# Kernel optimization log

Measured on AMD Instinct MI355X. Metric: run time of the kernel, lower is better.

## Reference

```python
import jax, jax.numpy as jnp
import numpy as np

H = 6  # num_heads
D = 384  # embedding_dim


def _rot(seg, coord):
    # seg: [BN, H, T, L], coord: [BN, T]; rotate interleaved even/odd pairs
    L = seg.shape[-1]
    pairs = max(L // 2, 1)
    inv_freq = 1.0 / (10000.0 ** (jnp.arange(pairs, dtype=seg.dtype) / pairs))
    ang = coord[..., None] * inv_freq          # [BN, T, pairs]
    cos = jnp.cos(ang)[:, None]                # [BN, 1, T, pairs]
    sin = jnp.sin(ang)[:, None]
    even, odd = seg[..., 0::2], seg[..., 1::2]
    re = even * cos - odd * sin
    ro = even * sin + odd * cos
    return jnp.stack((re, ro), axis=-1).reshape(seg.shape)


def _apply_rope3(t, pos, chunk):
    # t: [BN, H, T, Hd], pos: [BN, T, 3]; three axis chunks, tail untouched
    parts, s = [], 0
    for i in range(3):
        parts.append(_rot(t[..., s:s + chunk], pos[..., i]))
        s += chunk
    parts.append(t[..., s:])
    return jnp.concatenate(parts, axis=-1)


def setup_inputs() -> dict:
    key = jax.random.key(0)
    ks = jax.random.split(key, 10)
    B, N, T = 8, 64, 128
    scale = 1.0 / np.sqrt(D)
    return {
        "padded_batches": jax.random.normal(ks[0], (B, N, T, D), jnp.float32),
        "sum_token": jax.random.normal(ks[1], (B, N, 1, D), jnp.float32),
        "positions_3d": jax.random.uniform(ks[2], (B, N, T, 3), jnp.float32),
        "Wq": jax.random.normal(ks[3], (D, D), jnp.float32) * scale,
        "bq": jax.random.normal(ks[4], (D,), jnp.float32) * scale,
        "Wk": jax.random.normal(ks[5], (D, D), jnp.float32) * scale,
        "bk": jax.random.normal(ks[6], (D,), jnp.float32) * scale,
        "Wv": jax.random.normal(ks[7], (D, D), jnp.float32) * scale,
        "bv": jax.random.normal(ks[8], (D,), jnp.float32) * scale,
        "masks": jax.random.randint(ks[9], (B, N, T), 0, 2, jnp.int32),
    }


def reference(padded_batches, sum_token, positions_3d, Wq, bq, Wk, bk, Wv, bv, masks):
    B, N, T, Dm = padded_batches.shape
    Hd = Dm // H
    chunk = Hd // 6 * 2

    # masked mean-pool summary token (summary_mode='avg')
    w = masks[..., None].astype(padded_batches.dtype)          # [B,N,T,1]
    denom = jnp.clip(w.sum(axis=-2, keepdims=True), 1e-6, None)
    summary = (padded_batches * w).sum(axis=-2, keepdims=True) / denom  # [B,N,1,D]

    q = (padded_batches @ Wq + bq).reshape(B * N, T, H, Hd).transpose(0, 2, 1, 3)  # [BN,H,T,Hd]
    k = (summary @ Wk + bk).reshape(B * N, 1, H, Hd).transpose(0, 2, 1, 3)         # [BN,H,1,Hd]
    v = (summary @ Wv + bv).reshape(B * N, 1, H, Hd).transpose(0, 2, 1, 3)

    # 3-axis RoPE on q (token positions) and k (pooled positions)
    pos_summary = (positions_3d * w).sum(axis=-2, keepdims=True) / denom  # [B,N,1,3]
    pos_q = positions_3d.reshape(B * N, T, 3)
    pos_k = pos_summary.reshape(B * N, 1, 3)
    q = _apply_rope3(q, pos_q, chunk)
    k = _apply_rope3(k, pos_k, chunk)

    # SDPA with T queries vs 1 key
    scores = jnp.einsum('bhtd,bhkd->bhtk', q, k) / np.float32(np.sqrt(Hd))  # [BN,H,T,1]
    mask_add = jnp.where(masks.reshape(B * N, 1, T, 1) == 0,
                         jnp.finfo(jnp.float32).min, 0.0)
    attn_w = jax.nn.softmax(scores + mask_add, axis=-1)
    attn = jnp.einsum('bhtk,bhkd->bhtd', attn_w, v)  # [BN,H,T,Hd]

    out = attn.transpose(0, 2, 1, 3).reshape(B, N, T, Dm) + padded_batches
    return out
```

## Files before the change

### kernel.cpp

```cpp
#include <hip/hip_runtime.h>


#define DM 384
#define TT 128
#define C4 96
#define BN_TOT 512

typedef float f32x4 __attribute__((ext_vector_type(4)));

__device__ __forceinline__ void nt_store4(float4* p, const float4 v) {
    __builtin_nontemporal_store(*(const f32x4*)&v, (f32x4*)p);
}

__global__ __launch_bounds__(384) void k_partial(
    const float* __restrict__ padded,
    const int*   __restrict__ masks,
    float*       __restrict__ ws_part,
    float*       __restrict__ ws_cnt)
{
    const int b  = blockIdx.x;
    const int bn = b >> 2;
    const int q  = b & 3;
    const int t  = threadIdx.x;
    const int c  = t % C4;
    const int rr = t / C4;

    __shared__ float  w_sh[32];
    __shared__ float4 part[4][C4];

    if (t < 32) w_sh[t] = (float)masks[bn * TT + q * 32 + t];
    __syncthreads();

    const float4* __restrict__ p4 =
        (const float4*)padded + (size_t)bn * TT * C4 + (size_t)q * 32 * C4;

    float4 acc = make_float4(0.f, 0.f, 0.f, 0.f);
    #pragma unroll
    for (int j = 0; j < 8; ++j) {
        const int   r = rr + 4 * j;
        const float w = w_sh[r];
        const float4 x = p4[r * C4 + c];
        acc.x += x.x * w; acc.y += x.y * w; acc.z += x.z * w; acc.w += x.w * w;
    }
    part[rr][c] = acc;
    __syncthreads();

    if (t < C4) {
        const float4 a0 = part[0][t], a1 = part[1][t];
        const float4 a2 = part[2][t], a3 = part[3][t];
        float4 s;
        s.x = (a0.x + a1.x) + (a2.x + a3.x);
        s.y = (a0.y + a1.y) + (a2.y + a3.y);
        s.z = (a0.z + a1.z) + (a2.z + a3.z);
        s.w = (a0.w + a1.w) + (a2.w + a3.w);
        ((float4*)(ws_part + ((size_t)bn * 4 + q) * DM))[t] = s;
    } else if (t == C4) {
        float s0 = 0.f, s1 = 0.f, s2 = 0.f, s3 = 0.f;
        #pragma unroll
        for (int i = 0; i < 8; ++i) {
            s0 += w_sh[i];      s1 += w_sh[8 + i];
            s2 += w_sh[16 + i]; s3 += w_sh[24 + i];
        }
        ws_cnt[bn * 4 + q] = (s0 + s1) + (s2 + s3);
    }
}

__global__ __launch_bounds__(384) void k_final_add(
    const float* __restrict__ padded,
    const float* __restrict__ ws_part,
    const float* __restrict__ ws_cnt,
    const float* __restrict__ Wv,
    const float* __restrict__ bv,
    float*       __restrict__ out)
{
    const int b  = blockIdx.x;
    const int bn = b >> 1;
    const int h  = b & 1;
    const int t  = threadIdx.x;
    const int c4 = t % 48;
    const int g8 = t / 48;

    __shared__ float  summ[DM];
    __shared__ float4 mpart[8][48];
    __shared__ float4 v_sh[48];

    {
        const float* __restrict__ pp = ws_part + (size_t)bn * 4 * DM;
        const float  s = (pp[t] + pp[DM + t]) + (pp[2 * DM + t] + pp[3 * DM + t]);
        const float* __restrict__ cc = ws_cnt + bn * 4;
        const float  cnt = (cc[0] + cc[1]) + (cc[2] + cc[3]);
        summ[t] = s * (1.0f / fmaxf(cnt, 1e-6f));
    }
    __syncthreads();

    {
        float4 a = make_float4(0.f, 0.f, 0.f, 0.f);
        const float4* __restrict__ wv4 = (const float4*)Wv;
        #pragma unroll 6
        for (int j = 0; j < 48; ++j) {
            const int   e = g8 * 48 + j;
            const float s = summ[e];
            const float4 w = wv4[(size_t)e * C4 + h * 48 + c4];
            a.x += s * w.x; a.y += s * w.y; a.z += s * w.z; a.w += s * w.w;
        }
        mpart[g8][c4] = a;
    }
    __syncthreads();

    if (t < 48) {
        float4 v = ((const float4*)bv)[h * 48 + t];
        #pragma unroll
        for (int g = 0; g < 8; ++g) {
            const float4 p = mpart[g][t];
            v.x += p.x; v.y += p.y; v.z += p.z; v.w += p.w;
        }
        v_sh[t] = v;
    }
    __syncthreads();

    const float4* __restrict__ p4 = (const float4*)padded + (size_t)bn * TT * C4;
    float4*       __restrict__ o4 = (float4*)out + (size_t)bn * TT * C4;
    const float4 v = v_sh[c4];
    #pragma unroll
    for (int j = 0; j < 16; ++j) {
        const int    r   = g8 + 8 * j;
        const size_t idx = (size_t)r * C4 + h * 48 + c4;
        float4 x = p4[idx];
        x.x += v.x; x.y += v.y; x.z += v.z; x.w += v.w;
        nt_store4(&o4[idx], x);
    }
}

extern "C" void kernel_launch(void* const* d_in, const int* in_sizes, int n_in,
                              void* d_out, int out_size, void* d_ws, size_t ws_size,
                              hipStream_t stream) {
    const float* padded = (const float*)d_in[0];
    const float* Wv     = (const float*)d_in[7];
    const float* bv     = (const float*)d_in[8];
    const int*   masks  = (const int*)d_in[9];
    float* out = (float*)d_out;

    float* ws_part = (float*)d_ws;
    float* ws_cnt  = ws_part + (size_t)BN_TOT * 4 * DM;

    k_partial<<<BN_TOT * 4, 384, 0, stream>>>(padded, masks, ws_part, ws_cnt);
    k_final_add<<<BN_TOT * 2, 384, 0, stream>>>(padded, ws_part, ws_cnt,
                                                Wv, bv, out);
}
```

Measured before the change: 215.6 us.

## Fuse partial pooling and output add via last-block atomic counter

Merges the two kernels into one. Each of the four quarter-blocks for a sequence writes its partial masked sum, bumps an atomic counter, and the last block to arrive computes the summary, the V projection and the residual add for the whole sequence. Block indices are remapped so the four quarters of a sequence sit close together in launch order. This removes one kernel launch and the gap between launches, but adds a memset, atomics and fences, and leaves only a quarter of the blocks doing the full output pass serially.

```diff
diff --git a/kernel.cpp b/kernel.cpp
--- a/kernel.cpp
+++ b/kernel.cpp
@@ -5,6 +5,7 @@
 #define TT 128
 #define C4 96
 #define BN_TOT 512
+#define NBLK (BN_TOT * 4)
 
 typedef float f32x4 __attribute__((ext_vector_type(4)));
 
@@ -12,26 +13,34 @@
     __builtin_nontemporal_store(*(const f32x4*)&v, (f32x4*)p);
 }
 
-__global__ __launch_bounds__(384) void k_partial(
+__global__ __launch_bounds__(384) void fused_lastblock(
     const float* __restrict__ padded,
     const int*   __restrict__ masks,
-    float*       __restrict__ ws_part,
-    float*       __restrict__ ws_cnt)
+    const float* __restrict__ Wv,
+    const float* __restrict__ bv,
+    unsigned int* __restrict__ ws_cnt,
+    float*        __restrict__ ws_den,
+    float*        __restrict__ ws_part,
+    float*        __restrict__ out)
 {
-    const int b  = blockIdx.x;
-    const int bn = b >> 2;
-    const int q  = b & 3;
+    const int b = blockIdx.x;
+    const int q  = (b >> 3) & 3;
+    const int bn = ((b >> 5) << 3) | (b & 7);
+
     const int t  = threadIdx.x;
     const int c  = t % C4;
     const int rr = t / C4;
 
     __shared__ float  w_sh[32];
     __shared__ float4 part[4][C4];
+    __shared__ float  summ[DM];
+    __shared__ float  v_sh[DM];
+    __shared__ int    last_sh;
 
     if (t < 32) w_sh[t] = (float)masks[bn * TT + q * 32 + t];
     __syncthreads();
 
-    const float4* __restrict__ p4 =
+    const float4* __restrict__ p4q =
         (const float4*)padded + (size_t)bn * TT * C4 + (size_t)q * 32 * C4;
 
     float4 acc = make_float4(0.f, 0.f, 0.f, 0.f);
@@ -39,8 +48,9 @@
     for (int j = 0; j < 8; ++j) {
         const int   r = rr + 4 * j;
         const float w = w_sh[r];
-        const float4 x = p4[r * C4 + c];
-        acc.x += x.x * w; acc.y += x.y * w; acc.z += x.z * w; acc.w += x.w * w;
+        const float4 xv = p4q[r * C4 + c];
+        acc.x += xv.x * w; acc.y += xv.y * w;
+        acc.z += xv.z * w; acc.w += xv.w * w;
     }
     part[rr][c] = acc;
     __syncthreads();
@@ -61,73 +71,63 @@
             s0 += w_sh[i];      s1 += w_sh[8 + i];
             s2 += w_sh[16 + i]; s3 += w_sh[24 + i];
         }
-        ws_cnt[bn * 4 + q] = (s0 + s1) + (s2 + s3);
+        ws_den[bn * 4 + q] = (s0 + s1) + (s2 + s3);
     }
-}
 
-__global__ __launch_bounds__(384) void k_final_add(
-    const float* __restrict__ padded,
-    const float* __restrict__ ws_part,
-    const float* __restrict__ ws_cnt,
-    const float* __restrict__ Wv,
-    const float* __restrict__ bv,
-    float*       __restrict__ out)
-{
-    const int b  = blockIdx.x;
-    const int bn = b >> 1;
-    const int h  = b & 1;
-    const int t  = threadIdx.x;
-    const int c4 = t % 48;
-    const int g8 = t / 48;
+    __threadfence();
+    __syncthreads();
+    if (t == 0) {
+        const unsigned int old = atomicAdd(&ws_cnt[bn], 1u);
+        last_sh = (old == 3u);
+    }
+    __syncthreads();
+    if (!last_sh) return;
 
-    __shared__ float  summ[DM];
-    __shared__ float4 mpart[8][48];
-    __shared__ float4 v_sh[48];
+    __threadfence();
 
     {
         const float* __restrict__ pp = ws_part + (size_t)bn * 4 * DM;
         const float  s = (pp[t] + pp[DM + t]) + (pp[2 * DM + t] + pp[3 * DM + t]);
-        const float* __restrict__ cc = ws_cnt + bn * 4;
-        const float  cnt = (cc[0] + cc[1]) + (cc[2] + cc[3]);
-        summ[t] = s * (1.0f / fmaxf(cnt, 1e-6f));
+        const float* __restrict__ dd = ws_den + bn * 4;
+        const float  den = (dd[0] + dd[1]) + (dd[2] + dd[3]);
+        summ[t] = s * (1.0f / fmaxf(den, 1e-6f));
     }
     __syncthreads();
 
     {
         float4 a = make_float4(0.f, 0.f, 0.f, 0.f);
         const float4* __restrict__ wv4 = (const float4*)Wv;
-        #pragma unroll 6
-        for (int j = 0; j < 48; ++j) {
-            const int   e = g8 * 48 + j;
+        #pragma unroll 8
+        for (int j = 0; j < 96; ++j) {
+            const int   e = rr * 96 + j;
             const float s = summ[e];
-            const float4 w = wv4[(size_t)e * C4 + h * 48 + c4];
+            const float4 w = wv4[(size_t)e * C4 + c];
             a.x += s * w.x; a.y += s * w.y; a.z += s * w.z; a.w += s * w.w;
         }
-        mpart[g8][c4] = a;
+        part[rr][c] = a;
     }
     __syncthreads();
 
-    if (t < 48) {
-        float4 v = ((const float4*)bv)[h * 48 + t];
+    if (t < C4) {
+        float4 v = ((const float4*)bv)[t];
         #pragma unroll
-        for (int g = 0; g < 8; ++g) {
-            const float4 p = mpart[g][t];
+        for (int g = 0; g < 4; ++g) {
+            const float4 p = part[g][t];
             v.x += p.x; v.y += p.y; v.z += p.z; v.w += p.w;
         }
-        v_sh[t] = v;
+        ((float4*)v_sh)[t] = v;
     }
     __syncthreads();
 
     const float4* __restrict__ p4 = (const float4*)padded + (size_t)bn * TT * C4;
     float4*       __restrict__ o4 = (float4*)out + (size_t)bn * TT * C4;
-    const float4 v = v_sh[c4];
+    const float4 v = ((const float4*)v_sh)[c];
     #pragma unroll
-    for (int j = 0; j < 16; ++j) {
-        const int    r   = g8 + 8 * j;
-        const size_t idx = (size_t)r * C4 + h * 48 + c4;
-        float4 x = p4[idx];
-        x.x += v.x; x.y += v.y; x.z += v.z; x.w += v.w;
-        nt_store4(&o4[idx], x);
+    for (int j = 0; j < 32; ++j) {
+        const int r = rr + 4 * j;
+        float4 xv = p4[r * C4 + c];
+        xv.x += v.x; xv.y += v.y; xv.z += v.z; xv.w += v.w;
+        nt_store4(&o4[r * C4 + c], xv);
     }
 }
 
@@ -140,10 +140,11 @@
     const int*   masks  = (const int*)d_in[9];
     float* out = (float*)d_out;
 
-    float* ws_part = (float*)d_ws;
-    float* ws_cnt  = ws_part + (size_t)BN_TOT * 4 * DM;
+    unsigned int* ws_cnt = (unsigned int*)d_ws;
+    float* ws_den  = (float*)d_ws + BN_TOT;
+    float* ws_part = ws_den + (size_t)BN_TOT * 4;
 
-    k_partial<<<BN_TOT * 4, 384, 0, stream>>>(padded, masks, ws_part, ws_cnt);
-    k_final_add<<<BN_TOT * 2, 384, 0, stream>>>(padded, ws_part, ws_cnt,
-                                                Wv, bv, out);
+    hipMemsetAsync(ws_cnt, 0, BN_TOT * sizeof(unsigned int), stream);
+    fused_lastblock<<<NBLK, 384, 0, stream>>>(padded, masks, Wv, bv,
+                                              ws_cnt, ws_den, ws_part, out);
 }
```

New measurement: 792.0 us. 3.67x slower.
